# Performance work log

Measured on AMD Instinct MI355X. Metric: run time of the kernel, lower is better.

## Reference

```python
import jax, jax.numpy as jnp
import numpy as np

DIM = 64
PATCH = 8
KH = KW = 7
K = KH * KW
PAD = 3


def conv2d(x, w, pad):
    return jax.lax.conv_general_dilated(
        x, w, window_strides=(1, 1), padding=[(pad, pad), (pad, pad)],
        dimension_numbers=('NCHW', 'OIHW', 'NCHW'))


def deform_conv2d(x, offset, mask, weight):
    # torchvision modulated deformable conv v2, stride=1, dilation=1, pad=PAD
    B, C, H, W = x.shape
    off = offset.reshape(B, K, 2, H, W)  # channel pairs are (dy, dx)
    ky, kx = jnp.meshgrid(jnp.arange(KH), jnp.arange(KW), indexing='ij')
    ky = ky.reshape(K).astype(x.dtype)
    kx = kx.reshape(K).astype(x.dtype)
    hh = jnp.arange(H, dtype=x.dtype)
    ww = jnp.arange(W, dtype=x.dtype)
    # sampling locations: p0 - pad + p_k + offset, shape [B,K,H,W]
    y = hh[None, None, :, None] - PAD + ky[None, :, None, None] + off[:, :, 0]
    xx = ww[None, None, None, :] - PAD + kx[None, :, None, None] + off[:, :, 1]

    y0 = jnp.floor(y)
    x0 = jnp.floor(xx)
    wy = y - y0
    wx = xx - x0

    img_flat = x.reshape(B, C, H * W)

    def gather(yi, xi):
        valid = (yi >= 0) & (yi < H) & (xi >= 0) & (xi < W)
        yc = jnp.clip(yi, 0, H - 1).astype(jnp.int32)
        xc = jnp.clip(xi, 0, W - 1).astype(jnp.int32)
        lin = (yc * W + xc).reshape(B, -1)  # [B, K*H*W]
        v = jax.vmap(lambda im, idx: im[:, idx])(img_flat, lin)  # [B,C,K*H*W]
        v = v.reshape(B, C, K, H, W)
        return v * valid[:, None].astype(x.dtype)

    val = ((1 - wy) * (1 - wx))[:, None] * gather(y0, x0) \
        + ((1 - wy) * wx)[:, None] * gather(y0, x0 + 1) \
        + (wy * (1 - wx))[:, None] * gather(y0 + 1, x0) \
        + (wy * wx)[:, None] * gather(y0 + 1, x0 + 1)
    val = val * mask[:, None]  # modulation, [B,C,K,H,W]
    wf = weight.reshape(weight.shape[0], weight.shape[1], K)
    return jnp.einsum('bckhw,ock->bohw', val, wf)


def setup_inputs() -> dict:
    key = jax.random.key(0)
    ks = jax.random.split(key, 12)
    B, C, H, W = 1, DIM, 192, 192
    s = 0.05
    return {
        'enc': jax.random.normal(ks[0], (B, C, H, W), jnp.float32),
        'dec': jax.random.normal(ks[1], (B, C, H, W), jnp.float32),
        'inverse_offset': jax.random.normal(ks[2], (B, 2 * K, H, W), jnp.float32),
        'inverse_weight': jax.random.uniform(ks[3], (B, K, H, W), jnp.float32),
        'w_proj_in': jax.random.normal(ks[4], (C, C, 1, 1), jnp.float32) * s,
        'fft_w': 1.0 + 0.1 * jax.random.normal(ks[5], (C, 1, 1, PATCH, PATCH // 2 + 1), jnp.float32),
        'w_proj_out': jax.random.normal(ks[6], (2 * C, 2 * C, 1, 1), jnp.float32) * s,
        'w_deform': jax.random.normal(ks[7], (C, C, KH, KW), jnp.float32) * s,
        'w_conv1': jax.random.normal(ks[8], (C, C, 1, 1), jnp.float32) * s,
        'w_conv2': jax.random.normal(ks[9], (C, C, 3, 3), jnp.float32) * s,
    }


def reference(enc, dec, inverse_offset, inverse_weight, w_proj_in, fft_w,
              w_proj_out, w_deform, w_conv1, w_conv2):
    B, C, h, w = enc.shape
    reverse = deform_conv2d(enc, inverse_offset, inverse_weight, w_deform)
    reverse = conv2d(reverse, w_conv1, 0)

    e = conv2d(enc, w_proj_in, 0)
    # check_image_size: pad H,W to multiples of PATCH (no-op for 192)
    ph = (-h) % PATCH
    pw = (-w) % PATCH
    e = jnp.pad(e, ((0, 0), (0, 0), (0, ph), (0, pw)))
    Hp, Wp = h + ph, w + pw
    # [B,C,h',w',p1,p2]
    xp = e.reshape(B, C, Hp // PATCH, PATCH, Wp // PATCH, PATCH).transpose(0, 1, 2, 4, 3, 5)
    xf = jnp.fft.rfft2(xp.astype(jnp.float32)) * fft_w  # fft_w [C,1,1,8,5] broadcasts
    xp = jnp.fft.irfft2(xf, s=(PATCH, PATCH))
    e = xp.transpose(0, 1, 2, 4, 3, 5).reshape(B, C, Hp, Wp)[:, :, :h, :w]

    e = e + reverse
    e = conv2d(e, w_conv2, 1)
    feat = jnp.concatenate([e, dec], axis=1)
    feat = conv2d(feat, w_proj_out, 0)
    x1, x2 = jnp.split(feat, 2, axis=1)  # SimpleGate
    return x1 * x2
```

## Files before the change

kernel.cpp:

```cpp
#include <hip/hip_runtime.h>
#include <math.h>

#define CH    64
#define WW    192
#define HH    192
#define HWSZ  (192*192)
#define KK    49
#define ROWP  68
#define SROW  72
#define C3ROW 72
#define OROW  136

typedef __attribute__((ext_vector_type(8))) short     s16x8;
typedef __attribute__((ext_vector_type(8))) _Float16  h16x8;
typedef __attribute__((ext_vector_type(2))) _Float16  h16x2;
typedef __attribute__((ext_vector_type(2))) __fp16    fp16x2;
typedef __attribute__((ext_vector_type(4))) float     f32x4;

__device__ __forceinline__ unsigned short f2h(float f) {
    union { _Float16 h; unsigned short s; } u; u.h = (_Float16)f;
    return u.s;
}

__device__ __forceinline__ float h2f(unsigned short s) {
    union { unsigned short s; _Float16 h; } u; u.s = s;
    return (float)u.h;
}

__device__ __forceinline__ unsigned pkh(float lo, float hi) {
    union { fp16x2 h; unsigned u; } v;
    v.h = __builtin_amdgcn_cvt_pkrtz(lo, hi);
    return v.u;
}

__device__ __forceinline__ h16x2 cvt2h(float a) {
    union { fp16x2 h; h16x2 o; } v;
    v.h = __builtin_amdgcn_cvt_pkrtz(a, a);
    return v.o;
}

__device__ __forceinline__ h16x2 as_h2(unsigned u) {
    union { unsigned u; h16x2 h; } v; v.u = u; return v.h;
}

__device__ __forceinline__ unsigned as_u(h16x2 h) {
    union { h16x2 h; unsigned u; } v; v.h = h; return v.u;
}

__device__ const float c_cos8[8] = {
    1.f, 0.70710678118654752f, 0.f, -0.70710678118654752f,
   -1.f, -0.70710678118654752f, 0.f, 0.70710678118654752f };

__global__ __launch_bounds__(256) void k_pt(
    const float* __restrict__ enc,
    unsigned short* __restrict__ encH,
    const float* __restrict__ fw,
    const float* __restrict__ wd,
    const float* __restrict__ w2,
    const float* __restrict__ wc1,
    const float* __restrict__ wpo,
    const float* __restrict__ wpi,
    float* __restrict__ krT,
    short* __restrict__ wA,
    short* __restrict__ w2A,
    short* __restrict__ wpoA,
    short* __restrict__ wpiA)
{
    __shared__ __align__(16) char smem_raw[2 * 64 * ROWP * 4];
    int b = blockIdx.x;
    int t = threadIdx.x;

    if (b < 576) {
        float* s = (float*)smem_raw;
        int base = b * 64;
#pragma unroll
        for (int r = 0; r < 16; r++) {
            int idx = t + r * 256;
            int p = idx & 63, c = idx >> 6;
            s[p * 65 + c] = enc[c * HWSZ + base + p];
        }
        __syncthreads();
#pragma unroll
        for (int r = 0; r < 8; r++) {
            int idx = t + r * 256;
            int pr = idx & 31, p = idx >> 5;
            ((unsigned*)encH)[(base + p) * 32 + pr] =
                pkh(s[p * 65 + 2 * pr], s[p * 65 + 2 * pr + 1]);
        }
        return;
    }

    int kb = b - 576;
    int tid = kb * 256 + t;
    int nt  = 49 * 256;
    for (int u = tid; u < 64 * 64; u += nt) {
        int uv = u >> 6, c = u & 63;
        int uu = uv >> 3, v = uv & 7;
        float acc = 0.f;
        for (int ky = 0; ky < 8; ky++)
            for (int kx = 0; kx < 8; kx++) {
                float wv = (kx <= 4) ? fw[c * 40 + ky * 5 + kx]
                                     : fw[c * 40 + ((8 - ky) & 7) * 5 + (8 - kx)];
                acc += wv * c_cos8[(ky * uu + kx * v) & 7];
            }
        krT[uv * 64 + c] = acc * (1.f / 64.f);
    }
    for (int u = tid; u < 9 * 4096; u += nt) {
        int tap = u / 4096, rem = u & 4095;
        int o = rem >> 6, c = rem & 63;
        float v = w2[(o * 64 + c) * 9 + tap];
        int fi = tap * 8 + (o >> 4) * 2 + (c >> 5);
        int ln = ((c >> 3) & 3) * 16 + (o & 15);
        w2A[fi * 512 + ln * 8 + (c & 7)] = (short)f2h(v);
    }
    for (int u = tid; u < 128 * 128; u += nt) {
        int o = u >> 7, c = u & 127;
        int fi = (o >> 4) * 4 + (c >> 5);
        int ln = ((c >> 3) & 3) * 16 + (o & 15);
        wpoA[fi * 512 + ln * 8 + (c & 7)] = (short)f2h(wpo[u]);
    }
    for (int u = tid; u < 64 * 64; u += nt) {
        int o = u >> 6, c = u & 63;
        int fi = (o >> 4) * 2 + (c >> 5);
        int ln = ((c >> 3) & 3) * 16 + (o & 15);
        wpiA[fi * 512 + ln * 8 + (c & 7)] = (short)f2h(wpi[u]);
    }

    float* wdk  = (float*)smem_raw;
    float* wc1s = wdk + 64 * ROWP;
#pragma unroll
    for (int r = 0; r < 16; r++) {
        int idx = t + r * 256;
        int o = idx >> 6, c = idx & 63;
        wdk [o * ROWP + c] = wd[(o * 64 + c) * KK + kb];
        wc1s[o * ROWP + c] = wc1[o * 64 + c];
    }
    __syncthreads();

    int ot = (t >> 4) * 4, cb = (t & 15) * 4;
    float a[4][4];
#pragma unroll
    for (int i = 0; i < 4; i++)
#pragma unroll
        for (int j = 0; j < 4; j++) a[i][j] = 0.f;
    for (int o = 0; o < 64; o++) {
        float wv_[4], sv_[4];
#pragma unroll
        for (int i = 0; i < 4; i++) wv_[i] = wc1s[(ot + i) * ROWP + o];
#pragma unroll
        for (int j = 0; j < 4; j++) sv_[j] = wdk[o * ROWP + cb + j];
#pragma unroll
        for (int i = 0; i < 4; i++)
#pragma unroll
            for (int j = 0; j < 4; j++) a[i][j] += wv_[i] * sv_[j];
    }
#pragma unroll
    for (int i = 0; i < 4; i++)
#pragma unroll
        for (int j = 0; j < 4; j++) {
            int o2 = ot + i, c = cb + j;
            int tt = o2 >> 4, m = o2 & 15;
            int kt = c >> 5, q = (c >> 3) & 3, jj = c & 7;
            int ln = q * 16 + m;
            wA[(kb * 8 + tt * 2 + kt) * 512 + ln * 8 + jj] = (short)f2h(a[i][j]);
        }
}

#define REDW 20

__global__ __launch_bounds__(256) void k_dff(
    const unsigned short* __restrict__ encH, const float* __restrict__ off,
    const float* __restrict__ msk, const short* __restrict__ wA,
    unsigned short* __restrict__ revH,
    const short* __restrict__ wpiA, const float* __restrict__ krT,
    unsigned short* __restrict__ e1H)
{
    __shared__ __align__(16) char smem_raw[19456];
    int t = threadIdx.x;
    int lane = t & 63, w = t >> 6;
    int b = blockIdx.x;

    if (b < 2304) {
        short* sm_base = (short*)smem_raw;
        float* red = (float*)(smem_raw + 4 * 16 * SROW * 2);

        int xcd = b & 7, blk = b >> 3;
        int gy  = xcd * 24 + blk / 12;
        int gx0 = (blk % 12) * 16;

        int sp = lane >> 2, g = lane & 3;
        int sgx  = gx0 + sp;
        int gp_s = gy * WW + sgx;
        int n = lane & 15, q = lane >> 4;
        short* smw = sm_base + w * (16 * SROW);

        f32x4 acc[4];
#pragma unroll
        for (int ot = 0; ot < 4; ot++) acc[ot] = (f32x4){0.f, 0.f, 0.f, 0.f};

        int kstart = (w == 0) ? 0 : 13 + (w - 1) * 12;
        int kend   = (w == 0) ? 13 : kstart + 12;

        float dy = off[(2 * kstart) * HWSZ + gp_s];
        float dx = off[(2 * kstart + 1) * HWSZ + gp_s];
        float mm = msk[kstart * HWSZ + gp_s];

#pragma unroll 1
        for (int k = kstart; k < kend; k++) {
            int ky = k / 7, kx = k % 7;
            float y = (float)(gy  - 3 + ky) + dy;
            float x = (float)(sgx - 3 + kx) + dx;
            float y0f = floorf(y), x0f = floorf(x);
            float wy = y - y0f, wx = x - x0f;
            int iy0 = (int)y0f, ix0 = (int)x0f;
            int iy1 = iy0 + 1, ix1 = ix0 + 1;
            bool vy0 = (iy0 >= 0) & (iy0 < HH);
            bool vy1 = (iy1 >= 0) & (iy1 < HH);
            bool vx0 = (ix0 >= 0) & (ix0 < WW);
            bool vx1 = (ix1 >= 0) & (ix1 < WW);
            int iy0c = min(max(iy0, 0), HH - 1), iy1c = min(max(iy1, 0), HH - 1);
            int ix0c = min(max(ix0, 0), WW - 1), ix1c = min(max(ix1, 0), WW - 1);
            float a00 = (vy0 & vx0) ? (1.f - wy) * (1.f - wx) * mm : 0.f;
            float a01 = (vy0 & vx1) ? (1.f - wy) * wx * mm : 0.f;
            float a10 = (vy1 & vx0) ? wy * (1.f - wx) * mm : 0.f;
            float a11 = (vy1 & vx1) ? wy * wx * mm : 0.f;

            const unsigned short* b00p = encH + (iy0c * WW + ix0c) * 64 + g * 16;
            const unsigned short* b01p = encH + (iy0c * WW + ix1c) * 64 + g * 16;
            const unsigned short* b10p = encH + (iy1c * WW + ix0c) * 64 + g * 16;
            const unsigned short* b11p = encH + (iy1c * WW + ix1c) * 64 + g * 16;
            uint4 u00[2], u01[2], u10[2], u11[2];
            u00[0] = *(const uint4*)b00p;  u00[1] = *(const uint4*)(b00p + 8);
            u01[0] = *(const uint4*)b01p;  u01[1] = *(const uint4*)(b01p + 8);
            u10[0] = *(const uint4*)b10p;  u10[1] = *(const uint4*)(b10p + 8);
            u11[0] = *(const uint4*)b11p;  u11[1] = *(const uint4*)(b11p + 8);

            float dyn = 0.f, dxn = 0.f, mmn = 0.f;
            if (k + 1 < kend) {
                dyn = off[(2 * k + 2) * HWSZ + gp_s];
                dxn = off[(2 * k + 3) * HWSZ + gp_s];
                mmn = msk[(k + 1) * HWSZ + gp_s];
            }

            h16x8 af[8];
#pragma unroll
            for (int f = 0; f < 8; f++)
                af[f] = *(const h16x8*)&wA[(k * 8 + f) * 512 + lane * 8];

            h16x2 w00 = cvt2h(a00);
            h16x2 w01 = cvt2h(a01);
            h16x2 w10 = cvt2h(a10);
            h16x2 w11 = cvt2h(a11);

            unsigned c00[8] = {u00[0].x, u00[0].y, u00[0].z, u00[0].w,
                               u00[1].x, u00[1].y, u00[1].z, u00[1].w};
            unsigned c01[8] = {u01[0].x, u01[0].y, u01[0].z, u01[0].w,
                               u01[1].x, u01[1].y, u01[1].z, u01[1].w};
            unsigned c10[8] = {u10[0].x, u10[0].y, u10[0].z, u10[0].w,
                               u10[1].x, u10[1].y, u10[1].z, u10[1].w};
            unsigned c11[8] = {u11[0].x, u11[0].y, u11[0].z, u11[0].w,
                               u11[1].x, u11[1].y, u11[1].z, u11[1].w};
            unsigned pk[8];
#pragma unroll
            for (int j = 0; j < 8; j++) {
                h16x2 r = as_h2(c00[j]) * w00;
                r = as_h2(c01[j]) * w01 + r;
                r = as_h2(c10[j]) * w10 + r;
                r = as_h2(c11[j]) * w11 + r;
                pk[j] = as_u(r);
            }
            *(uint4*)&smw[sp * SROW + g * 16]     = make_uint4(pk[0], pk[1], pk[2], pk[3]);
            *(uint4*)&smw[sp * SROW + g * 16 + 8] = make_uint4(pk[4], pk[5], pk[6], pk[7]);

            h16x8 b0 = *(const h16x8*)&smw[n * SROW +  0 + q * 8];
            h16x8 b1 = *(const h16x8*)&smw[n * SROW + 32 + q * 8];

#pragma unroll
            for (int ot = 0; ot < 4; ot++) {
                acc[ot] = __builtin_amdgcn_mfma_f32_16x16x32_f16(af[ot * 2],     b0, acc[ot], 0, 0, 0);
                acc[ot] = __builtin_amdgcn_mfma_f32_16x16x32_f16(af[ot * 2 + 1], b1, acc[ot], 0, 0, 0);
            }

            dy = dyn; dx = dxn; mm = mmn;
        }

        if (w >= 2) {
            float* rp = &red[((w - 2) * 64 + lane) * REDW];
#pragma unroll
            for (int ot = 0; ot < 4; ot++)
                *(float4*)&rp[ot * 4] = make_float4(acc[ot][0], acc[ot][1], acc[ot][2], acc[ot][3]);
        }
        __syncthreads();
        if (w < 2) {
            const float* rp = &red[(w * 64 + lane) * REDW];
#pragma unroll
            for (int ot = 0; ot < 4; ot++) {
                float4 v = *(const float4*)&rp[ot * 4];
                acc[ot][0] += v.x; acc[ot][1] += v.y;
                acc[ot][2] += v.z; acc[ot][3] += v.w;
            }
        }
        __syncthreads();
        if (w == 1) {
            float* rp = &red[lane * REDW];
#pragma unroll
            for (int ot = 0; ot < 4; ot++)
                *(float4*)&rp[ot * 4] = make_float4(acc[ot][0], acc[ot][1], acc[ot][2], acc[ot][3]);
        }
        __syncthreads();
        if (w == 0) {
            const float* rp = &red[lane * REDW];
#pragma unroll
            for (int ot = 0; ot < 4; ot++) {
                float4 v = *(const float4*)&rp[ot * 4];
                acc[ot][0] += v.x; acc[ot][1] += v.y;
                acc[ot][2] += v.z; acc[ot][3] += v.w;
            }
            int gp_m = gy * WW + gx0 + n;
#pragma unroll
            for (int ot = 0; ot < 4; ot++) {
                unsigned u0 = pkh(acc[ot][0], acc[ot][1]);
                unsigned u1 = pkh(acc[ot][2], acc[ot][3]);
                *(uint2*)&revH[gp_m * 64 + ot * 16 + q * 4] = make_uint2(u0, u1);
            }
        }
        return;
    }

    {
        short* sbf = (short*)smem_raw;
        short* e0H = (short*)(smem_raw + 64 * SROW * 2);

        int pb = b - 2304;
        int pbx = pb % 24, pby = pb / 24;
        int gx0 = pbx * 8, gy0 = pby * 8;

#pragma unroll
        for (int r = 0; r < 2; r++) {
            int idx = t + r * 256;
            int px = idx >> 3, g8 = idx & 7;
            int gy = gy0 + (px >> 3), gx = gx0 + (px & 7);
            *(uint4*)&sbf[px * SROW + g8 * 8] =
                *(const uint4*)&encH[(gy * WW + gx) * 64 + g8 * 8];
        }
        __syncthreads();

        int n = lane & 15, q = lane >> 4;
        h16x8 a0 = *(const h16x8*)&wpiA[(w * 2 + 0) * 512 + lane * 8];
        h16x8 a1 = *(const h16x8*)&wpiA[(w * 2 + 1) * 512 + lane * 8];
#pragma unroll
        for (int j = 0; j < 4; j++) {
            h16x8 b0 = *(const h16x8*)&sbf[(j * 16 + n) * SROW +  0 + q * 8];
            h16x8 b1 = *(const h16x8*)&sbf[(j * 16 + n) * SROW + 32 + q * 8];
            f32x4 acc = {0.f, 0.f, 0.f, 0.f};
            acc = __builtin_amdgcn_mfma_f32_16x16x32_f16(a0, b0, acc, 0, 0, 0);
            acc = __builtin_amdgcn_mfma_f32_16x16x32_f16(a1, b1, acc, 0, 0, 0);
            unsigned u0 = pkh(acc[0], acc[1]);
            unsigned u1 = pkh(acc[2], acc[3]);
            *(unsigned*)&e0H[(j * 16 + n) * SROW + w * 16 + q * 4]     = u0;
            *(unsigned*)&e0H[(j * 16 + n) * SROW + w * 16 + q * 4 + 2] = u1;
        }
        __syncthreads();

        int o = t & 63;
        int yb = t >> 6;
#pragma unroll
        for (int yy = 0; yy < 2; yy++) {
            int y = yb + yy * 4;
            float outr[8];
#pragma unroll
            for (int x = 0; x < 8; x++) outr[x] = 0.f;
#pragma unroll
            for (int u = 0; u < 8; u++) {
                int ry = (y - u + 8) & 7;
                float row[8];
#pragma unroll
                for (int rx = 0; rx < 8; rx++)
                    row[rx] = h2f(((const unsigned short*)e0H)[(ry * 8 + rx) * SROW + o]);
#pragma unroll
                for (int v = 0; v < 8; v++) {
                    float kv = krT[(u * 8 + v) * 64 + o];
#pragma unroll
                    for (int x = 0; x < 8; x++)
                        outr[x] += kv * row[(x - v + 8) & 7];
                }
            }
            int gy = gy0 + y;
#pragma unroll
            for (int x = 0; x < 8; x++)
                e1H[(gy * WW + gx0 + x) * 64 + o] = f2h(outr[x]);
        }
    }
}

__global__ __launch_bounds__(256) void k_c3out(
    const unsigned short* __restrict__ e1H, const unsigned short* __restrict__ revH,
    const short* __restrict__ w2A, const float* __restrict__ dec,
    const short* __restrict__ wpoA, float* __restrict__ out)
{
    __shared__ __align__(16) short sm[4][54 * C3ROW];
    int t = threadIdx.x;
    int lane = t & 63, w = t >> 6;
    int b = blockIdx.x;
    int xcd = b & 7, blk = b >> 3;
    int gy  = xcd * 24 + blk / 3;
    int gx0 = (blk % 3) * 64 + w * 16;
    short* smw = &sm[w][0];
    int n = lane & 15, q = lane >> 4;

    for (int r = 0; r < 14; r++) {
        int u = lane + r * 64;
        if (u < 864) {
            int rp = u >> 4, g = u & 15;
            int row = rp / 18, pxl = rp - row * 18;
            int gyy = gy + row - 1, gxx = gx0 + pxl - 1;
            uint2 v = make_uint2(0u, 0u);
            if (gyy >= 0 && gyy < HH && gxx >= 0 && gxx < WW) {
                int gp = (gyy * WW + gxx) * 64 + g * 4;
                uint2 va = *(const uint2*)&e1H[gp];
                uint2 vb = *(const uint2*)&revH[gp];
                v.x = as_u(as_h2(va.x) + as_h2(vb.x));
                v.y = as_u(as_h2(va.y) + as_h2(vb.y));
            }
            *(uint2*)&smw[rp * C3ROW + g * 4] = v;
        }
    }

    f32x4 acc[4];
#pragma unroll
    for (int ot = 0; ot < 4; ot++) acc[ot] = (f32x4){0.f, 0.f, 0.f, 0.f};

#pragma unroll 1
    for (int tap = 0; tap < 9; tap++) {
        int dy = tap / 3, dx = tap - dy * 3;
        int rp = dy * 18 + n + dx;
        h16x8 b0 = *(const h16x8*)&smw[rp * C3ROW +  0 + q * 8];
        h16x8 b1 = *(const h16x8*)&smw[rp * C3ROW + 32 + q * 8];
#pragma unroll
        for (int ot = 0; ot < 4; ot++) {
            h16x8 a0 = *(const h16x8*)&w2A[(tap * 8 + ot * 2 + 0) * 512 + lane * 8];
            h16x8 a1 = *(const h16x8*)&w2A[(tap * 8 + ot * 2 + 1) * 512 + lane * 8];
            acc[ot] = __builtin_amdgcn_mfma_f32_16x16x32_f16(a0, b0, acc[ot], 0, 0, 0);
            acc[ot] = __builtin_amdgcn_mfma_f32_16x16x32_f16(a1, b1, acc[ot], 0, 0, 0);
        }
    }

#pragma unroll
    for (int ot = 0; ot < 4; ot++) {
        unsigned lo = pkh(acc[ot][0], acc[ot][1]);
        unsigned hi = pkh(acc[ot][2], acc[ot][3]);
        *(uint2*)&smw[n * OROW + ot * 16 + q * 4] = make_uint2(lo, hi);
    }
    {
        int gp = gy * WW + gx0 + n;
        unsigned pk[8];
#pragma unroll
        for (int i = 0; i < 8; i++) {
            float va = dec[(q * 16 + 2 * i)     * HWSZ + gp];
            float vb = dec[(q * 16 + 2 * i + 1) * HWSZ + gp];
            pk[i] = pkh(va, vb);
        }
        *(uint4*)&smw[n * OROW + 64 + q * 16]     = make_uint4(pk[0], pk[1], pk[2], pk[3]);
        *(uint4*)&smw[n * OROW + 64 + q * 16 + 8] = make_uint4(pk[4], pk[5], pk[6], pk[7]);
    }

    f32x4 go[8];
#pragma unroll
    for (int ot = 0; ot < 8; ot++) go[ot] = (f32x4){0.f, 0.f, 0.f, 0.f};

#pragma unroll 1
    for (int kt = 0; kt < 4; kt++) {
        h16x8 bb = *(const h16x8*)&smw[n * OROW + kt * 32 + q * 8];
#pragma unroll
        for (int ot = 0; ot < 8; ot++) {
            h16x8 aa = *(const h16x8*)&wpoA[(ot * 4 + kt) * 512 + lane * 8];
            go[ot] = __builtin_amdgcn_mfma_f32_16x16x32_f16(aa, bb, go[ot], 0, 0, 0);
        }
    }

    int gp = gy * WW + gx0 + n;
#pragma unroll
    for (int ot = 0; ot < 4; ot++)
#pragma unroll
        for (int r = 0; r < 4; r++)
            out[(ot * 16 + q * 4 + r) * HWSZ + gp] = go[ot][r] * go[ot + 4][r];
}

extern "C" void kernel_launch(void* const* d_in, const int* in_sizes, int n_in,
                              void* d_out, int out_size, void* d_ws, size_t ws_size,
                              hipStream_t stream)
{
    const float* enc  = (const float*)d_in[0];
    const float* dec  = (const float*)d_in[1];
    const float* ioff = (const float*)d_in[2];
    const float* iwt  = (const float*)d_in[3];
    const float* wpi  = (const float*)d_in[4];
    const float* fw   = (const float*)d_in[5];
    const float* wpo  = (const float*)d_in[6];
    const float* wd   = (const float*)d_in[7];
    const float* wc1  = (const float*)d_in[8];
    const float* wc2  = (const float*)d_in[9];
    float* out = (float*)d_out;
    float* ws  = (float*)d_ws;

    float*          krT  = ws;
    unsigned short* revH = (unsigned short*)(ws + 4096);
    unsigned short* e1H  = (unsigned short*)(ws + 1183744);
    unsigned short* encH = (unsigned short*)(ws + 2363392);
    short*          wA   = (short*)(ws + 3543040);
    short*          w2A  = (short*)(ws + 3643392);
    short*          wpoA = (short*)(ws + 3661824);
    short*          wpiA = (short*)(ws + 3670016);

    hipLaunchKernelGGL(k_pt,    dim3(625),  dim3(256), 0, stream,
                       enc, encH, fw, wd, wc2, wc1, wpo, wpi, krT, wA, w2A, wpoA, wpiA);
    hipLaunchKernelGGL(k_dff,   dim3(2880), dim3(256), 0, stream,
                       encH, ioff, iwt, wA, revH, wpiA, krT, e1H);
    hipLaunchKernelGGL(k_c3out, dim3(576),  dim3(256), 0, stream,
                       e1H, revH, w2A, dec, wpoA, out);
}
```

Measured before the change: 189.8 us.

## Merge three kernels into one persistent kernel with grid-wide barriers

Replaces the three separate launches (preprocess, deformable+FFT stage, conv3+output stage) with a single persistent kernel of 768 blocks. Global atomic-counter barriers sit between the stages, and the middle stage loops over the former 2880 work items. The aim is to remove launch gaps and tail idle time between kernels. The cost is spin-wait barrier overhead, an extra memset, and a dependence on all 768 blocks being co-resident (launch_bounds 256,4). The shared-memory row padding was also dropped (ROWP 68 to 64), which may add bank conflicts.

```diff
diff --git a/kernel.cpp b/kernel.cpp
--- a/kernel.cpp
+++ b/kernel.cpp
@@ -6,10 +6,11 @@
 #define HH    192
 #define HWSZ  (192*192)
 #define KK    49
-#define ROWP  68
 #define SROW  72
 #define C3ROW 72
 #define OROW  136
+#define REDW  20
+#define GRID  768
 
 typedef __attribute__((ext_vector_type(8))) short     s16x8;
 typedef __attribute__((ext_vector_type(8))) _Float16  h16x8;
@@ -51,7 +52,18 @@
     1.f, 0.70710678118654752f, 0.f, -0.70710678118654752f,
    -1.f, -0.70710678118654752f, 0.f, 0.70710678118654752f };
 
-__global__ __launch_bounds__(256) void k_pt(
+__device__ __forceinline__ void gbar(int* cnt) {
+    __threadfence();
+    __syncthreads();
+    if (threadIdx.x == 0) {
+        atomicAdd(cnt, 1);
+        while (atomicAdd(cnt, 0) < GRID) __builtin_amdgcn_s_sleep(32);
+    }
+    __syncthreads();
+    __threadfence();
+}
+
+__global__ __launch_bounds__(256, 4) void k_all(
     const float* __restrict__ enc,
     unsigned short* __restrict__ encH,
     const float* __restrict__ fw,
@@ -64,11 +76,19 @@
     short* __restrict__ wA,
     short* __restrict__ w2A,
     short* __restrict__ wpoA,
-    short* __restrict__ wpiA)
+    short* __restrict__ wpiA,
+    const float* __restrict__ off,
+    const float* __restrict__ msk,
+    unsigned short* __restrict__ revH,
+    unsigned short* __restrict__ e1H,
+    const float* __restrict__ dec,
+    float* __restrict__ out,
+    int* gcnt)
 {
-    __shared__ __align__(16) char smem_raw[2 * 64 * ROWP * 4];
+    __shared__ __align__(16) char smem_raw[32768];
     int b = blockIdx.x;
     int t = threadIdx.x;
+    int lane = t & 63, w = t >> 6;
 
     if (b < 576) {
         float* s = (float*)smem_raw;
@@ -87,403 +107,385 @@
             ((unsigned*)encH)[(base + p) * 32 + pr] =
                 pkh(s[p * 65 + 2 * pr], s[p * 65 + 2 * pr + 1]);
         }
-        return;
+    } else if (b < 625) {
+        int kb = b - 576;
+        int tid = kb * 256 + t;
+        int nt  = 49 * 256;
+        for (int u = tid; u < 64 * 64; u += nt) {
+            int uv = u >> 6, c = u & 63;
+            int uu = uv >> 3, v = uv & 7;
+            float acc = 0.f;
+            for (int ky = 0; ky < 8; ky++)
+                for (int kx = 0; kx < 8; kx++) {
+                    float wv = (kx <= 4) ? fw[c * 40 + ky * 5 + kx]
+                                         : fw[c * 40 + ((8 - ky) & 7) * 5 + (8 - kx)];
+                    acc += wv * c_cos8[(ky * uu + kx * v) & 7];
+                }
+            krT[uv * 64 + c] = acc * (1.f / 64.f);
+        }
+        for (int u = tid; u < 9 * 4096; u += nt) {
+            int tap = u / 4096, rem = u & 4095;
+            int o = rem >> 6, c = rem & 63;
+            float v = w2[(o * 64 + c) * 9 + tap];
+            int fi = tap * 8 + (o >> 4) * 2 + (c >> 5);
+            int ln = ((c >> 3) & 3) * 16 + (o & 15);
+            w2A[fi * 512 + ln * 8 + (c & 7)] = (short)f2h(v);
+        }
+        for (int u = tid; u < 128 * 128; u += nt) {
+            int o = u >> 7, c = u & 127;
+            int fi = (o >> 4) * 4 + (c >> 5);
+            int ln = ((c >> 3) & 3) * 16 + (o & 15);
+            wpoA[fi * 512 + ln * 8 + (c & 7)] = (short)f2h(wpo[u]);
+        }
+        for (int u = tid; u < 64 * 64; u += nt) {
+            int o = u >> 6, c = u & 63;
+            int fi = (o >> 4) * 2 + (c >> 5);
+            int ln = ((c >> 3) & 3) * 16 + (o & 15);
+            wpiA[fi * 512 + ln * 8 + (c & 7)] = (short)f2h(wpi[u]);
+        }
+
+        float* wdk  = (float*)smem_raw;
+        float* wc1s = wdk + 4096;
+#pragma unroll
+        for (int r = 0; r < 16; r++) {
+            int idx = t + r * 256;
+            int o = idx >> 6, c = idx & 63;
+            wdk [o * 64 + c] = wd[(o * 64 + c) * KK + kb];
+            wc1s[o * 64 + c] = wc1[o * 64 + c];
+        }
+        __syncthreads();
+
+        int ot = (t >> 4) * 4, cb = (t & 15) * 4;
+        float a[4][4];
+#pragma unroll
+        for (int i = 0; i < 4; i++)
+#pragma unroll
+            for (int j = 0; j < 4; j++) a[i][j] = 0.f;
+        for (int o = 0; o < 64; o++) {
+            float wv_[4], sv_[4];
+#pragma unroll
+            for (int i = 0; i < 4; i++) wv_[i] = wc1s[(ot + i) * 64 + o];
+#pragma unroll
+            for (int j = 0; j < 4; j++) sv_[j] = wdk[o * 64 + cb + j];
+#pragma unroll
+            for (int i = 0; i < 4; i++)
+#pragma unroll
+                for (int j = 0; j < 4; j++) a[i][j] += wv_[i] * sv_[j];
+        }
+#pragma unroll
+        for (int i = 0; i < 4; i++)
+#pragma unroll
+            for (int j = 0; j < 4; j++) {
+                int o2 = ot + i, c = cb + j;
+                int tt = o2 >> 4, m = o2 & 15;
+                int kt = c >> 5, q2 = (c >> 3) & 3, jj = c & 7;
+                int ln = q2 * 16 + m;
+                wA[(kb * 8 + tt * 2 + kt) * 512 + ln * 8 + jj] = (short)f2h(a[i][j]);
+            }
     }
 
-    int kb = b - 576;
-    int tid = kb * 256 + t;
-    int nt  = 49 * 256;
-    for (int u = tid; u < 64 * 64; u += nt) {
-        int uv = u >> 6, c = u & 63;
-        int uu = uv >> 3, v = uv & 7;
-        float acc = 0.f;
-        for (int ky = 0; ky < 8; ky++)
-            for (int kx = 0; kx < 8; kx++) {
-                float wv = (kx <= 4) ? fw[c * 40 + ky * 5 + kx]
-                                     : fw[c * 40 + ((8 - ky) & 7) * 5 + (8 - kx)];
-                acc += wv * c_cos8[(ky * uu + kx * v) & 7];
-            }
-        krT[uv * 64 + c] = acc * (1.f / 64.f);
+    gbar(gcnt + 0);
+
+#pragma unroll 1
+    for (int ub = b; ub < 2880; ub += GRID) {
+        __syncthreads();
+        if (ub < 2304) {
+            short* sm_base = (short*)smem_raw;
+            float* red = (float*)(smem_raw + 4 * 16 * SROW * 2);
+
+            int xcd = ub & 7, blk = ub >> 3;
+            int gy  = xcd * 24 + blk / 12;
+            int gx0 = (blk % 12) * 16;
+
+            int sp = lane >> 2, g = lane & 3;
+            int sgx  = gx0 + sp;
+            int gp_s = gy * WW + sgx;
+            int n = lane & 15, q = lane >> 4;
+            short* smw = sm_base + w * (16 * SROW);
+
+            f32x4 acc[4];
+#pragma unroll
+            for (int ot = 0; ot < 4; ot++) acc[ot] = (f32x4){0.f, 0.f, 0.f, 0.f};
+
+            int kstart = (w == 0) ? 0 : 13 + (w - 1) * 12;
+            int kend   = (w == 0) ? 13 : kstart + 12;
+
+            float dy = off[(2 * kstart) * HWSZ + gp_s];
+            float dx = off[(2 * kstart + 1) * HWSZ + gp_s];
+            float mm = msk[kstart * HWSZ + gp_s];
+
+#pragma unroll 1
+            for (int k = kstart; k < kend; k++) {
+                int ky = k / 7, kx = k % 7;
+                float y = (float)(gy  - 3 + ky) + dy;
+                float x = (float)(sgx - 3 + kx) + dx;
+                float y0f = floorf(y), x0f = floorf(x);
+                float wy = y - y0f, wx = x - x0f;
+                int iy0 = (int)y0f, ix0 = (int)x0f;
+                int iy1 = iy0 + 1, ix1 = ix0 + 1;
+                bool vy0 = (iy0 >= 0) & (iy0 < HH);
+                bool vy1 = (iy1 >= 0) & (iy1 < HH);
+                bool vx0 = (ix0 >= 0) & (ix0 < WW);
+                bool vx1 = (ix1 >= 0) & (ix1 < WW);
+                int iy0c = min(max(iy0, 0), HH - 1), iy1c = min(max(iy1, 0), HH - 1);
+                int ix0c = min(max(ix0, 0), WW - 1), ix1c = min(max(ix1, 0), WW - 1);
+                float a00 = (vy0 & vx0) ? (1.f - wy) * (1.f - wx) * mm : 0.f;
+                float a01 = (vy0 & vx1) ? (1.f - wy) * wx * mm : 0.f;
+                float a10 = (vy1 & vx0) ? wy * (1.f - wx) * mm : 0.f;
+                float a11 = (vy1 & vx1) ? wy * wx * mm : 0.f;
+
+                const unsigned short* b00p = encH + (iy0c * WW + ix0c) * 64 + g * 16;
+                const unsigned short* b01p = encH + (iy0c * WW + ix1c) * 64 + g * 16;
+                const unsigned short* b10p = encH + (iy1c * WW + ix0c) * 64 + g * 16;
+                const unsigned short* b11p = encH + (iy1c * WW + ix1c) * 64 + g * 16;
+                uint4 u00[2], u01[2], u10[2], u11[2];
+                u00[0] = *(const uint4*)b00p;  u00[1] = *(const uint4*)(b00p + 8);
+                u01[0] = *(const uint4*)b01p;  u01[1] = *(const uint4*)(b01p + 8);
+                u10[0] = *(const uint4*)b10p;  u10[1] = *(const uint4*)(b10p + 8);
+                u11[0] = *(const uint4*)b11p;  u11[1] = *(const uint4*)(b11p + 8);
+
+                float dyn = 0.f, dxn = 0.f, mmn = 0.f;
+                if (k + 1 < kend) {
+                    dyn = off[(2 * k + 2) * HWSZ + gp_s];
+                    dxn = off[(2 * k + 3) * HWSZ + gp_s];
+                    mmn = msk[(k + 1) * HWSZ + gp_s];
+                }
+
+                h16x8 af[8];
+#pragma unroll
+                for (int f = 0; f < 8; f++)
+                    af[f] = *(const h16x8*)&wA[(k * 8 + f) * 512 + lane * 8];
+
+                h16x2 w00 = cvt2h(a00);
+                h16x2 w01 = cvt2h(a01);
+                h16x2 w10 = cvt2h(a10);
+                h16x2 w11 = cvt2h(a11);
+
+                unsigned c00[8] = {u00[0].x, u00[0].y, u00[0].z, u00[0].w,
+                                   u00[1].x, u00[1].y, u00[1].z, u00[1].w};
+                unsigned c01[8] = {u01[0].x, u01[0].y, u01[0].z, u01[0].w,
+                                   u01[1].x, u01[1].y, u01[1].z, u01[1].w};
+                unsigned c10[8] = {u10[0].x, u10[0].y, u10[0].z, u10[0].w,
+                                   u10[1].x, u10[1].y, u10[1].z, u10[1].w};
+                unsigned c11[8] = {u11[0].x, u11[0].y, u11[0].z, u11[0].w,
+                                   u11[1].x, u11[1].y, u11[1].z, u11[1].w};
+                unsigned pk[8];
+#pragma unroll
+                for (int j = 0; j < 8; j++) {
+                    h16x2 r = as_h2(c00[j]) * w00;
+                    r = as_h2(c01[j]) * w01 + r;
+                    r = as_h2(c10[j]) * w10 + r;
+                    r = as_h2(c11[j]) * w11 + r;
+                    pk[j] = as_u(r);
+                }
+                *(uint4*)&smw[sp * SROW + g * 16]     = make_uint4(pk[0], pk[1], pk[2], pk[3]);
+                *(uint4*)&smw[sp * SROW + g * 16 + 8] = make_uint4(pk[4], pk[5], pk[6], pk[7]);
+
+                h16x8 b0 = *(const h16x8*)&smw[n * SROW +  0 + q * 8];
+                h16x8 b1 = *(const h16x8*)&smw[n * SROW + 32 + q * 8];
+
+#pragma unroll
+                for (int ot = 0; ot < 4; ot++) {
+                    acc[ot] = __builtin_amdgcn_mfma_f32_16x16x32_f16(af[ot * 2],     b0, acc[ot], 0, 0, 0);
+                    acc[ot] = __builtin_amdgcn_mfma_f32_16x16x32_f16(af[ot * 2 + 1], b1, acc[ot], 0, 0, 0);
+                }
+
+                dy = dyn; dx = dxn; mm = mmn;
+            }
+
+            if (w >= 2) {
+                float* rp = &red[((w - 2) * 64 + lane) * REDW];
+#pragma unroll
+                for (int ot = 0; ot < 4; ot++)
+                    *(float4*)&rp[ot * 4] = make_float4(acc[ot][0], acc[ot][1], acc[ot][2], acc[ot][3]);
+            }
+            __syncthreads();
+            if (w < 2) {
+                const float* rp = &red[(w * 64 + lane) * REDW];
+#pragma unroll
+                for (int ot = 0; ot < 4; ot++) {
+                    float4 v = *(const float4*)&rp[ot * 4];
+                    acc[ot][0] += v.x; acc[ot][1] += v.y;
+                    acc[ot][2] += v.z; acc[ot][3] += v.w;
+                }
+            }
+            __syncthreads();
+            if (w == 1) {
+                float* rp = &red[lane * REDW];
+#pragma unroll
+                for (int ot = 0; ot < 4; ot++)
+                    *(float4*)&rp[ot * 4] = make_float4(acc[ot][0], acc[ot][1], acc[ot][2], acc[ot][3]);
+            }
+            __syncthreads();
+            if (w == 0) {
+                const float* rp = &red[lane * REDW];
+#pragma unroll
+                for (int ot = 0; ot < 4; ot++) {
+                    float4 v = *(const float4*)&rp[ot * 4];
+                    acc[ot][0] += v.x; acc[ot][1] += v.y;
+                    acc[ot][2] += v.z; acc[ot][3] += v.w;
+                }
+                int gp_m = gy * WW + gx0 + n;
+#pragma unroll
+                for (int ot = 0; ot < 4; ot++) {
+                    unsigned u0 = pkh(acc[ot][0], acc[ot][1]);
+                    unsigned u1 = pkh(acc[ot][2], acc[ot][3]);
+                    *(uint2*)&revH[gp_m * 64 + ot * 16 + q * 4] = make_uint2(u0, u1);
+                }
+            }
+        } else {
+            short* sbf = (short*)smem_raw;
+            short* e0H = (short*)(smem_raw + 64 * SROW * 2);
+
+            int pb = ub - 2304;
+            int pbx = pb % 24, pby = pb / 24;
+            int gx0 = pbx * 8, gy0 = pby * 8;
+
+#pragma unroll
+            for (int r = 0; r < 2; r++) {
+                int idx = t + r * 256;
+                int px = idx >> 3, g8 = idx & 7;
+                int gy = gy0 + (px >> 3), gx = gx0 + (px & 7);
+                *(uint4*)&sbf[px * SROW + g8 * 8] =
+                    *(const uint4*)&encH[(gy * WW + gx) * 64 + g8 * 8];
+            }
+            __syncthreads();
+
+            int n = lane & 15, q = lane >> 4;
+            h16x8 a0 = *(const h16x8*)&wpiA[(w * 2 + 0) * 512 + lane * 8];
+            h16x8 a1 = *(const h16x8*)&wpiA[(w * 2 + 1) * 512 + lane * 8];
+#pragma unroll
+            for (int j = 0; j < 4; j++) {
+                h16x8 b0 = *(const h16x8*)&sbf[(j * 16 + n) * SROW +  0 + q * 8];
+                h16x8 b1 = *(const h16x8*)&sbf[(j * 16 + n) * SROW + 32 + q * 8];
+                f32x4 acc = {0.f, 0.f, 0.f, 0.f};
+                acc = __builtin_amdgcn_mfma_f32_16x16x32_f16(a0, b0, acc, 0, 0, 0);
+                acc = __builtin_amdgcn_mfma_f32_16x16x32_f16(a1, b1, acc, 0, 0, 0);
+                unsigned u0 = pkh(acc[0], acc[1]);
+                unsigned u1 = pkh(acc[2], acc[3]);
+                *(unsigned*)&e0H[(j * 16 + n) * SROW + w * 16 + q * 4]     = u0;
+                *(unsigned*)&e0H[(j * 16 + n) * SROW + w * 16 + q * 4 + 2] = u1;
+            }
+            __syncthreads();
+
+            int o = t & 63;
+            int yb = t >> 6;
+#pragma unroll
+            for (int yy = 0; yy < 2; yy++) {
+                int y = yb + yy * 4;
+                float outr[8];
+#pragma unroll
+                for (int x = 0; x < 8; x++) outr[x] = 0.f;
+#pragma unroll
+                for (int u = 0; u < 8; u++) {
+                    int ry = (y - u + 8) & 7;
+                    float row[8];
+#pragma unroll
+                    for (int rx = 0; rx < 8; rx++)
+                        row[rx] = h2f(((const unsigned short*)e0H)[(ry * 8 + rx) * SROW + o]);
+#pragma unroll
+                    for (int v = 0; v < 8; v++) {
+                        float kv = krT[(u * 8 + v) * 64 + o];
+#pragma unroll
+                        for (int x = 0; x < 8; x++)
+                            outr[x] += kv * row[(x - v + 8) & 7];
+                    }
+                }
+                int gy = gy0 + y;
+#pragma unroll
+                for (int x = 0; x < 8; x++)
+                    e1H[(gy * WW + gx0 + x) * 64 + o] = f2h(outr[x]);
+            }
+        }
     }
-    for (int u = tid; u < 9 * 4096; u += nt) {
-        int tap = u / 4096, rem = u & 4095;
-        int o = rem >> 6, c = rem & 63;
-        float v = w2[(o * 64 + c) * 9 + tap];
-        int fi = tap * 8 + (o >> 4) * 2 + (c >> 5);
-        int ln = ((c >> 3) & 3) * 16 + (o & 15);
-        w2A[fi * 512 + ln * 8 + (c & 7)] = (short)f2h(v);
+
+    gbar(gcnt + 1);
+
+    if (b < 576) {
+        short* sm = (short*)smem_raw;
+        int xcd = b & 7, blk = b >> 3;
+        int gy  = xcd * 24 + blk / 3;
+        int gx0 = (blk % 3) * 64 + w * 16;
+        short* smw = sm + w * (54 * C3ROW);
+        int n = lane & 15, q = lane >> 4;
+
+        for (int r = 0; r < 14; r++) {
+            int u = lane + r * 64;
+            if (u < 864) {
+                int rp = u >> 4, g = u & 15;
+                int row = rp / 18, pxl = rp - row * 18;
+                int gyy = gy + row - 1, gxx = gx0 + pxl - 1;
+                uint2 v = make_uint2(0u, 0u);
+                if (gyy >= 0 && gyy < HH && gxx >= 0 && gxx < WW) {
+                    int gp = (gyy * WW + gxx) * 64 + g * 4;
+                    uint2 va = *(const uint2*)&e1H[gp];
+                    uint2 vb = *(const uint2*)&revH[gp];
+                    v.x = as_u(as_h2(va.x) + as_h2(vb.x));
+                    v.y = as_u(as_h2(va.y) + as_h2(vb.y));
+                }
+                *(uint2*)&smw[rp * C3ROW + g * 4] = v;
+            }
+        }
+
+        f32x4 acc[4];
+#pragma unroll
+        for (int ot = 0; ot < 4; ot++) acc[ot] = (f32x4){0.f, 0.f, 0.f, 0.f};
+
+#pragma unroll 1
+        for (int tap = 0; tap < 9; tap++) {
+            int dy = tap / 3, dx = tap - dy * 3;
+            int rp = dy * 18 + n + dx;
+            h16x8 b0 = *(const h16x8*)&smw[rp * C3ROW +  0 + q * 8];
+            h16x8 b1 = *(const h16x8*)&smw[rp * C3ROW + 32 + q * 8];
+#pragma unroll
+            for (int ot = 0; ot < 4; ot++) {
+                h16x8 a0 = *(const h16x8*)&w2A[(tap * 8 + ot * 2 + 0) * 512 + lane * 8];
+                h16x8 a1 = *(const h16x8*)&w2A[(tap * 8 + ot * 2 + 1) * 512 + lane * 8];
+                acc[ot] = __builtin_amdgcn_mfma_f32_16x16x32_f16(a0, b0, acc[ot], 0, 0, 0);
+                acc[ot] = __builtin_amdgcn_mfma_f32_16x16x32_f16(a1, b1, acc[ot], 0, 0, 0);
+            }
+        }
+
+#pragma unroll
+        for (int ot = 0; ot < 4; ot++) {
+            unsigned lo = pkh(acc[ot][0], acc[ot][1]);
+            unsigned hi = pkh(acc[ot][2], acc[ot][3]);
+            *(uint2*)&smw[n * OROW + ot * 16 + q * 4] = make_uint2(lo, hi);
+        }
+        {
+            int gp = gy * WW + gx0 + n;
+            unsigned pk[8];
+#pragma unroll
+            for (int i = 0; i < 8; i++) {
+                float va = dec[(q * 16 + 2 * i)     * HWSZ + gp];
+                float vb = dec[(q * 16 + 2 * i + 1) * HWSZ + gp];
+                pk[i] = pkh(va, vb);
+            }
+            *(uint4*)&smw[n * OROW + 64 + q * 16]     = make_uint4(pk[0], pk[1], pk[2], pk[3]);
+            *(uint4*)&smw[n * OROW + 64 + q * 16 + 8] = make_uint4(pk[4], pk[5], pk[6], pk[7]);
+        }
+
+        f32x4 go[8];
+#pragma unroll
+        for (int ot = 0; ot < 8; ot++) go[ot] = (f32x4){0.f, 0.f, 0.f, 0.f};
+
+#pragma unroll 1
+        for (int kt = 0; kt < 4; kt++) {
+            h16x8 bb = *(const h16x8*)&smw[n * OROW + kt * 32 + q * 8];
+#pragma unroll
+            for (int ot = 0; ot < 8; ot++) {
+                h16x8 aa = *(const h16x8*)&wpoA[(ot * 4 + kt) * 512 + lane * 8];
+                go[ot] = __builtin_amdgcn_mfma_f32_16x16x32_f16(aa, bb, go[ot], 0, 0, 0);
+            }
+        }
+
+        int gp = gy * WW + gx0 + n;
+#pragma unroll
+        for (int ot = 0; ot < 4; ot++)
+#pragma unroll
+            for (int r = 0; r < 4; r++)
+                out[(ot * 16 + q * 4 + r) * HWSZ + gp] = go[ot][r] * go[ot + 4][r];
     }
-    for (int u = tid; u < 128 * 128; u += nt) {
-        int o = u >> 7, c = u & 127;
-        int fi = (o >> 4) * 4 + (c >> 5);
-        int ln = ((c >> 3) & 3) * 16 + (o & 15);
-        wpoA[fi * 512 + ln * 8 + (c & 7)] = (short)f2h(wpo[u]);
-    }
-    for (int u = tid; u < 64 * 64; u += nt) {
-        int o = u >> 6, c = u & 63;
-        int fi = (o >> 4) * 2 + (c >> 5);
-        int ln = ((c >> 3) & 3) * 16 + (o & 15);
-        wpiA[fi * 512 + ln * 8 + (c & 7)] = (short)f2h(wpi[u]);
-    }
-
-    float* wdk  = (float*)smem_raw;
-    float* wc1s = wdk + 64 * ROWP;
-#pragma unroll
-    for (int r = 0; r < 16; r++) {
-        int idx = t + r * 256;
-        int o = idx >> 6, c = idx & 63;
-        wdk [o * ROWP + c] = wd[(o * 64 + c) * KK + kb];
-        wc1s[o * ROWP + c] = wc1[o * 64 + c];
-    }
-    __syncthreads();
-
-    int ot = (t >> 4) * 4, cb = (t & 15) * 4;
-    float a[4][4];
-#pragma unroll
-    for (int i = 0; i < 4; i++)
-#pragma unroll
-        for (int j = 0; j < 4; j++) a[i][j] = 0.f;
-    for (int o = 0; o < 64; o++) {
-        float wv_[4], sv_[4];
-#pragma unroll
-        for (int i = 0; i < 4; i++) wv_[i] = wc1s[(ot + i) * ROWP + o];
-#pragma unroll
-        for (int j = 0; j < 4; j++) sv_[j] = wdk[o * ROWP + cb + j];
-#pragma unroll
-        for (int i = 0; i < 4; i++)
-#pragma unroll
-            for (int j = 0; j < 4; j++) a[i][j] += wv_[i] * sv_[j];
-    }
-#pragma unroll
-    for (int i = 0; i < 4; i++)
-#pragma unroll
-        for (int j = 0; j < 4; j++) {
-            int o2 = ot + i, c = cb + j;
-            int tt = o2 >> 4, m = o2 & 15;
-            int kt = c >> 5, q = (c >> 3) & 3, jj = c & 7;
-            int ln = q * 16 + m;
-            wA[(kb * 8 + tt * 2 + kt) * 512 + ln * 8 + jj] = (short)f2h(a[i][j]);
-        }
-}
-
-#define REDW 20
-
-__global__ __launch_bounds__(256) void k_dff(
-    const unsigned short* __restrict__ encH, const float* __restrict__ off,
-    const float* __restrict__ msk, const short* __restrict__ wA,
-    unsigned short* __restrict__ revH,
-    const short* __restrict__ wpiA, const float* __restrict__ krT,
-    unsigned short* __restrict__ e1H)
-{
-    __shared__ __align__(16) char smem_raw[19456];
-    int t = threadIdx.x;
-    int lane = t & 63, w = t >> 6;
-    int b = blockIdx.x;
-
-    if (b < 2304) {
-        short* sm_base = (short*)smem_raw;
-        float* red = (float*)(smem_raw + 4 * 16 * SROW * 2);
-
-        int xcd = b & 7, blk = b >> 3;
-        int gy  = xcd * 24 + blk / 12;
-        int gx0 = (blk % 12) * 16;
-
-        int sp = lane >> 2, g = lane & 3;
-        int sgx  = gx0 + sp;
-        int gp_s = gy * WW + sgx;
-        int n = lane & 15, q = lane >> 4;
-        short* smw = sm_base + w * (16 * SROW);
-
-        f32x4 acc[4];
-#pragma unroll
-        for (int ot = 0; ot < 4; ot++) acc[ot] = (f32x4){0.f, 0.f, 0.f, 0.f};
-
-        int kstart = (w == 0) ? 0 : 13 + (w - 1) * 12;
-        int kend   = (w == 0) ? 13 : kstart + 12;
-
-        float dy = off[(2 * kstart) * HWSZ + gp_s];
-        float dx = off[(2 * kstart + 1) * HWSZ + gp_s];
-        float mm = msk[kstart * HWSZ + gp_s];
-
-#pragma unroll 1
-        for (int k = kstart; k < kend; k++) {
-            int ky = k / 7, kx = k % 7;
-            float y = (float)(gy  - 3 + ky) + dy;
-            float x = (float)(sgx - 3 + kx) + dx;
-            float y0f = floorf(y), x0f = floorf(x);
-            float wy = y - y0f, wx = x - x0f;
-            int iy0 = (int)y0f, ix0 = (int)x0f;
-            int iy1 = iy0 + 1, ix1 = ix0 + 1;
-            bool vy0 = (iy0 >= 0) & (iy0 < HH);
-            bool vy1 = (iy1 >= 0) & (iy1 < HH);
-            bool vx0 = (ix0 >= 0) & (ix0 < WW);
-            bool vx1 = (ix1 >= 0) & (ix1 < WW);
-            int iy0c = min(max(iy0, 0), HH - 1), iy1c = min(max(iy1, 0), HH - 1);
-            int ix0c = min(max(ix0, 0), WW - 1), ix1c = min(max(ix1, 0), WW - 1);
-            float a00 = (vy0 & vx0) ? (1.f - wy) * (1.f - wx) * mm : 0.f;
-            float a01 = (vy0 & vx1) ? (1.f - wy) * wx * mm : 0.f;
-            float a10 = (vy1 & vx0) ? wy * (1.f - wx) * mm : 0.f;
-            float a11 = (vy1 & vx1) ? wy * wx * mm : 0.f;
-
-            const unsigned short* b00p = encH + (iy0c * WW + ix0c) * 64 + g * 16;
-            const unsigned short* b01p = encH + (iy0c * WW + ix1c) * 64 + g * 16;
-            const unsigned short* b10p = encH + (iy1c * WW + ix0c) * 64 + g * 16;
-            const unsigned short* b11p = encH + (iy1c * WW + ix1c) * 64 + g * 16;
-            uint4 u00[2], u01[2], u10[2], u11[2];
-            u00[0] = *(const uint4*)b00p;  u00[1] = *(const uint4*)(b00p + 8);
-            u01[0] = *(const uint4*)b01p;  u01[1] = *(const uint4*)(b01p + 8);
-            u10[0] = *(const uint4*)b10p;  u10[1] = *(const uint4*)(b10p + 8);
-            u11[0] = *(const uint4*)b11p;  u11[1] = *(const uint4*)(b11p + 8);
-
-            float dyn = 0.f, dxn = 0.f, mmn = 0.f;
-            if (k + 1 < kend) {
-                dyn = off[(2 * k + 2) * HWSZ + gp_s];
-                dxn = off[(2 * k + 3) * HWSZ + gp_s];
-                mmn = msk[(k + 1) * HWSZ + gp_s];
-            }
-
-            h16x8 af[8];
-#pragma unroll
-            for (int f = 0; f < 8; f++)
-                af[f] = *(const h16x8*)&wA[(k * 8 + f) * 512 + lane * 8];
-
-            h16x2 w00 = cvt2h(a00);
-            h16x2 w01 = cvt2h(a01);
-            h16x2 w10 = cvt2h(a10);
-            h16x2 w11 = cvt2h(a11);
-
-            unsigned c00[8] = {u00[0].x, u00[0].y, u00[0].z, u00[0].w,
-                               u00[1].x, u00[1].y, u00[1].z, u00[1].w};
-            unsigned c01[8] = {u01[0].x, u01[0].y, u01[0].z, u01[0].w,
-                               u01[1].x, u01[1].y, u01[1].z, u01[1].w};
-            unsigned c10[8] = {u10[0].x, u10[0].y, u10[0].z, u10[0].w,
-                               u10[1].x, u10[1].y, u10[1].z, u10[1].w};
-            unsigned c11[8] = {u11[0].x, u11[0].y, u11[0].z, u11[0].w,
-                               u11[1].x, u11[1].y, u11[1].z, u11[1].w};
-            unsigned pk[8];
-#pragma unroll
-            for (int j = 0; j < 8; j++) {
-                h16x2 r = as_h2(c00[j]) * w00;
-                r = as_h2(c01[j]) * w01 + r;
-                r = as_h2(c10[j]) * w10 + r;
-                r = as_h2(c11[j]) * w11 + r;
-                pk[j] = as_u(r);
-            }
-            *(uint4*)&smw[sp * SROW + g * 16]     = make_uint4(pk[0], pk[1], pk[2], pk[3]);
-            *(uint4*)&smw[sp * SROW + g * 16 + 8] = make_uint4(pk[4], pk[5], pk[6], pk[7]);
-
-            h16x8 b0 = *(const h16x8*)&smw[n * SROW +  0 + q * 8];
-            h16x8 b1 = *(const h16x8*)&smw[n * SROW + 32 + q * 8];
-
-#pragma unroll
-            for (int ot = 0; ot < 4; ot++) {
-                acc[ot] = __builtin_amdgcn_mfma_f32_16x16x32_f16(af[ot * 2],     b0, acc[ot], 0, 0, 0);
-                acc[ot] = __builtin_amdgcn_mfma_f32_16x16x32_f16(af[ot * 2 + 1], b1, acc[ot], 0, 0, 0);
-            }
-
-            dy = dyn; dx = dxn; mm = mmn;
-        }
-
-        if (w >= 2) {
-            float* rp = &red[((w - 2) * 64 + lane) * REDW];
-#pragma unroll
-            for (int ot = 0; ot < 4; ot++)
-                *(float4*)&rp[ot * 4] = make_float4(acc[ot][0], acc[ot][1], acc[ot][2], acc[ot][3]);
-        }
-        __syncthreads();
-        if (w < 2) {
-            const float* rp = &red[(w * 64 + lane) * REDW];
-#pragma unroll
-            for (int ot = 0; ot < 4; ot++) {
-                float4 v = *(const float4*)&rp[ot * 4];
-                acc[ot][0] += v.x; acc[ot][1] += v.y;
-                acc[ot][2] += v.z; acc[ot][3] += v.w;
-            }
-        }
-        __syncthreads();
-        if (w == 1) {
-            float* rp = &red[lane * REDW];
-#pragma unroll
-            for (int ot = 0; ot < 4; ot++)
-                *(float4*)&rp[ot * 4] = make_float4(acc[ot][0], acc[ot][1], acc[ot][2], acc[ot][3]);
-        }
-        __syncthreads();
-        if (w == 0) {
-            const float* rp = &red[lane * REDW];
-#pragma unroll
-            for (int ot = 0; ot < 4; ot++) {
-                float4 v = *(const float4*)&rp[ot * 4];
-                acc[ot][0] += v.x; acc[ot][1] += v.y;
-                acc[ot][2] += v.z; acc[ot][3] += v.w;
-            }
-            int gp_m = gy * WW + gx0 + n;
-#pragma unroll
-            for (int ot = 0; ot < 4; ot++) {
-                unsigned u0 = pkh(acc[ot][0], acc[ot][1]);
-                unsigned u1 = pkh(acc[ot][2], acc[ot][3]);
-                *(uint2*)&revH[gp_m * 64 + ot * 16 + q * 4] = make_uint2(u0, u1);
-            }
-        }
-        return;
-    }
-
-    {
-        short* sbf = (short*)smem_raw;
-        short* e0H = (short*)(smem_raw + 64 * SROW * 2);
-
-        int pb = b - 2304;
-        int pbx = pb % 24, pby = pb / 24;
-        int gx0 = pbx * 8, gy0 = pby * 8;
-
-#pragma unroll
-        for (int r = 0; r < 2; r++) {
-            int idx = t + r * 256;
-            int px = idx >> 3, g8 = idx & 7;
-            int gy = gy0 + (px >> 3), gx = gx0 + (px & 7);
-            *(uint4*)&sbf[px * SROW + g8 * 8] =
-                *(const uint4*)&encH[(gy * WW + gx) * 64 + g8 * 8];
-        }
-        __syncthreads();
-
-        int n = lane & 15, q = lane >> 4;
-        h16x8 a0 = *(const h16x8*)&wpiA[(w * 2 + 0) * 512 + lane * 8];
-        h16x8 a1 = *(const h16x8*)&wpiA[(w * 2 + 1) * 512 + lane * 8];
-#pragma unroll
-        for (int j = 0; j < 4; j++) {
-            h16x8 b0 = *(const h16x8*)&sbf[(j * 16 + n) * SROW +  0 + q * 8];
-            h16x8 b1 = *(const h16x8*)&sbf[(j * 16 + n) * SROW + 32 + q * 8];
-            f32x4 acc = {0.f, 0.f, 0.f, 0.f};
-            acc = __builtin_amdgcn_mfma_f32_16x16x32_f16(a0, b0, acc, 0, 0, 0);
-            acc = __builtin_amdgcn_mfma_f32_16x16x32_f16(a1, b1, acc, 0, 0, 0);
-            unsigned u0 = pkh(acc[0], acc[1]);
-            unsigned u1 = pkh(acc[2], acc[3]);
-            *(unsigned*)&e0H[(j * 16 + n) * SROW + w * 16 + q * 4]     = u0;
-            *(unsigned*)&e0H[(j * 16 + n) * SROW + w * 16 + q * 4 + 2] = u1;
-        }
-        __syncthreads();
-
-        int o = t & 63;
-        int yb = t >> 6;
-#pragma unroll
-        for (int yy = 0; yy < 2; yy++) {
-            int y = yb + yy * 4;
-            float outr[8];
-#pragma unroll
-            for (int x = 0; x < 8; x++) outr[x] = 0.f;
-#pragma unroll
-            for (int u = 0; u < 8; u++) {
-                int ry = (y - u + 8) & 7;
-                float row[8];
-#pragma unroll
-                for (int rx = 0; rx < 8; rx++)
-                    row[rx] = h2f(((const unsigned short*)e0H)[(ry * 8 + rx) * SROW + o]);
-#pragma unroll
-                for (int v = 0; v < 8; v++) {
-                    float kv = krT[(u * 8 + v) * 64 + o];
-#pragma unroll
-                    for (int x = 0; x < 8; x++)
-                        outr[x] += kv * row[(x - v + 8) & 7];
-                }
-            }
-            int gy = gy0 + y;
-#pragma unroll
-            for (int x = 0; x < 8; x++)
-                e1H[(gy * WW + gx0 + x) * 64 + o] = f2h(outr[x]);
-        }
-    }
-}
-
-__global__ __launch_bounds__(256) void k_c3out(
-    const unsigned short* __restrict__ e1H, const unsigned short* __restrict__ revH,
-    const short* __restrict__ w2A, const float* __restrict__ dec,
-    const short* __restrict__ wpoA, float* __restrict__ out)
-{
-    __shared__ __align__(16) short sm[4][54 * C3ROW];
-    int t = threadIdx.x;
-    int lane = t & 63, w = t >> 6;
-    int b = blockIdx.x;
-    int xcd = b & 7, blk = b >> 3;
-    int gy  = xcd * 24 + blk / 3;
-    int gx0 = (blk % 3) * 64 + w * 16;
-    short* smw = &sm[w][0];
-    int n = lane & 15, q = lane >> 4;
-
-    for (int r = 0; r < 14; r++) {
-        int u = lane + r * 64;
-        if (u < 864) {
-            int rp = u >> 4, g = u & 15;
-            int row = rp / 18, pxl = rp - row * 18;
-            int gyy = gy + row - 1, gxx = gx0 + pxl - 1;
-            uint2 v = make_uint2(0u, 0u);
-            if (gyy >= 0 && gyy < HH && gxx >= 0 && gxx < WW) {
-                int gp = (gyy * WW + gxx) * 64 + g * 4;
-                uint2 va = *(const uint2*)&e1H[gp];
-                uint2 vb = *(const uint2*)&revH[gp];
-                v.x = as_u(as_h2(va.x) + as_h2(vb.x));
-                v.y = as_u(as_h2(va.y) + as_h2(vb.y));
-            }
-            *(uint2*)&smw[rp * C3ROW + g * 4] = v;
-        }
-    }
-
-    f32x4 acc[4];
-#pragma unroll
-    for (int ot = 0; ot < 4; ot++) acc[ot] = (f32x4){0.f, 0.f, 0.f, 0.f};
-
-#pragma unroll 1
-    for (int tap = 0; tap < 9; tap++) {
-        int dy = tap / 3, dx = tap - dy * 3;
-        int rp = dy * 18 + n + dx;
-        h16x8 b0 = *(const h16x8*)&smw[rp * C3ROW +  0 + q * 8];
-        h16x8 b1 = *(const h16x8*)&smw[rp * C3ROW + 32 + q * 8];
-#pragma unroll
-        for (int ot = 0; ot < 4; ot++) {
-            h16x8 a0 = *(const h16x8*)&w2A[(tap * 8 + ot * 2 + 0) * 512 + lane * 8];
-            h16x8 a1 = *(const h16x8*)&w2A[(tap * 8 + ot * 2 + 1) * 512 + lane * 8];
-            acc[ot] = __builtin_amdgcn_mfma_f32_16x16x32_f16(a0, b0, acc[ot], 0, 0, 0);
-            acc[ot] = __builtin_amdgcn_mfma_f32_16x16x32_f16(a1, b1, acc[ot], 0, 0, 0);
-        }
-    }
-
-#pragma unroll
-    for (int ot = 0; ot < 4; ot++) {
-        unsigned lo = pkh(acc[ot][0], acc[ot][1]);
-        unsigned hi = pkh(acc[ot][2], acc[ot][3]);
-        *(uint2*)&smw[n * OROW + ot * 16 + q * 4] = make_uint2(lo, hi);
-    }
-    {
-        int gp = gy * WW + gx0 + n;
-        unsigned pk[8];
-#pragma unroll
-        for (int i = 0; i < 8; i++) {
-            float va = dec[(q * 16 + 2 * i)     * HWSZ + gp];
-            float vb = dec[(q * 16 + 2 * i + 1) * HWSZ + gp];
-            pk[i] = pkh(va, vb);
-        }
-        *(uint4*)&smw[n * OROW + 64 + q * 16]     = make_uint4(pk[0], pk[1], pk[2], pk[3]);
-        *(uint4*)&smw[n * OROW + 64 + q * 16 + 8] = make_uint4(pk[4], pk[5], pk[6], pk[7]);
-    }
-
-    f32x4 go[8];
-#pragma unroll
-    for (int ot = 0; ot < 8; ot++) go[ot] = (f32x4){0.f, 0.f, 0.f, 0.f};
-
-#pragma unroll 1
-    for (int kt = 0; kt < 4; kt++) {
-        h16x8 bb = *(const h16x8*)&smw[n * OROW + kt * 32 + q * 8];
-#pragma unroll
-        for (int ot = 0; ot < 8; ot++) {
-            h16x8 aa = *(const h16x8*)&wpoA[(ot * 4 + kt) * 512 + lane * 8];
-            go[ot] = __builtin_amdgcn_mfma_f32_16x16x32_f16(aa, bb, go[ot], 0, 0, 0);
-        }
-    }
-
-    int gp = gy * WW + gx0 + n;
-#pragma unroll
-    for (int ot = 0; ot < 4; ot++)
-#pragma unroll
-        for (int r = 0; r < 4; r++)
-            out[(ot * 16 + q * 4 + r) * HWSZ + gp] = go[ot][r] * go[ot + 4][r];
 }
 
 extern "C" void kernel_launch(void* const* d_in, const int* in_sizes, int n_in,
@@ -511,11 +513,10 @@
     short*          w2A  = (short*)(ws + 3643392);
     short*          wpoA = (short*)(ws + 3661824);
     short*          wpiA = (short*)(ws + 3670016);
-
-    hipLaunchKernelGGL(k_pt,    dim3(625),  dim3(256), 0, stream,
-                       enc, encH, fw, wd, wc2, wc1, wpo, wpi, krT, wA, w2A, wpoA, wpiA);
-    hipLaunchKernelGGL(k_dff,   dim3(2880), dim3(256), 0, stream,
-                       encH, ioff, iwt, wA, revH, wpiA, krT, e1H);
-    hipLaunchKernelGGL(k_c3out, dim3(576),  dim3(256), 0, stream,
-                       e1H, revH, w2A, dec, wpoA, out);
-}
+    int*            gcnt = (int*)(ws + 3680000);
+
+    hipMemsetAsync(gcnt, 0, 2 * sizeof(int), stream);
+    hipLaunchKernelGGL(k_all, dim3(GRID), dim3(256), 0, stream,
+                       enc, encH, fw, wd, wc2, wc1, wpo, wpi, krT, wA,
+                       w2A, wpoA, wpiA, ioff, iwt, revH, e1H, dec, out, gcnt);
+}
```

Result: slower. 599.0 us (+215.6%).
